# Kernel optimization log

Measured on AMD Instinct MI355X. Metric: run time of the kernel, lower is better.

Reference implementation:

```python
import jax, jax.numpy as jnp
import numpy as np
from math import sqrt

D = 512        # output_dim (layer_dims[-1])
H = 4          # num_heads
ATN = D // H   # atn_dim = 128
BERT_D = 768
B = 32         # number of graph pairs
NP = 4096
NH = 4096


def setup_inputs() -> dict:
    key = jax.random.key(0)
    ks = jax.random.split(key, 20)
    inp = {
        'ctx_p': jax.random.normal(ks[0], (NP, D), jnp.float32),
        'ctx_h': jax.random.normal(ks[1], (NH, D), jnp.float32),
        'lhs_p': jax.random.normal(ks[2], (NP, BERT_D), jnp.float32),
        'lhs_h': jax.random.normal(ks[3], (NH, BERT_D), jnp.float32),
        'batch_p': jnp.sort(jax.random.randint(ks[4], (NP,), 0, B)).astype(jnp.int64),
        'batch_h': jnp.sort(jax.random.randint(ks[5], (NH,), 0, B)).astype(jnp.int64),
        # learned parameters (stored [in, out])
        'Wq': jax.random.normal(ks[6], (D, D), jnp.float32) * 0.02,
        'bq': jnp.zeros((D,), jnp.float32),
        'Wk': jax.random.normal(ks[7], (D, D), jnp.float32) * 0.02,
        'bk': jnp.zeros((D,), jnp.float32),
        'Wv': jax.random.normal(ks[8], (BERT_D, BERT_D), jnp.float32) * 0.02,
        'bv': jnp.zeros((BERT_D,), jnp.float32),
        'W1': jax.random.normal(ks[9], (D + BERT_D, 256), jnp.float32) * 0.02,
        'b1': jnp.zeros((256,), jnp.float32),
        'W2': jax.random.normal(ks[10], (256, 128), jnp.float32) * 0.02,
        'ln_g': jnp.ones((128,), jnp.float32),
        'ln_b': jnp.zeros((128,), jnp.float32),
        'Wc': jax.random.normal(ks[11], (128, 3), jnp.float32) * 0.02,
        'bc': jnp.zeros((3,), jnp.float32),
    }
    return inp


def reference(ctx_p, ctx_h, lhs_p, lhs_h, batch_p, batch_h,
              Wq, bq, Wk, bk, Wv, bv, W1, b1, W2, ln_g, ln_b, Wc, bc):
    # q/k projections; torch code does .view(-1, atn_dim, num_heads) -> head is fastest axis
    qs = (ctx_h @ Wq + bq).reshape(-1, ATN, H)          # [nh, atn, H]
    ks = (ctx_p @ Wk + bk).reshape(-1, ATN, H)          # [np, atn, H]
    vs = (lhs_p @ Wv + bv).reshape(-1, H, BERT_D // H)  # [np, H, 768/H]

    atn = jnp.einsum('ndh,mdh->nmh', qs, ks) / sqrt(ATN)  # [nh, np, H]
    # faithful to original: positions where batch ids MATCH are set to -1e10
    mask_same = batch_h[:, None] == batch_p[None, :]       # [nh, np]
    atn = jnp.where(mask_same[:, :, None], jnp.float32(-1e10), atn)
    atn = jax.nn.softmax(atn, axis=1)                      # softmax over premise words m

    attended = jnp.einsum('nmh,mhd->nhd', atn, vs).reshape(-1, BERT_D)  # [nh, 768]

    feats = jnp.concatenate([ctx_h, lhs_h - attended], axis=1)  # [nh, D+768]
    h1 = jax.nn.gelu(feats @ W1 + b1, approximate=False)
    h2 = h1 @ W2                                                # Linear no bias
    mu = h2.mean(axis=-1, keepdims=True)
    var = ((h2 - mu) ** 2).mean(axis=-1, keepdims=True)
    h2 = (h2 - mu) * jax.lax.rsqrt(var + 1e-5) * ln_g + ln_b    # LayerNorm(128)

    # global_mean_pool over batch_h
    pooled = jax.ops.segment_sum(h2, batch_h, num_segments=B)
    counts = jax.ops.segment_sum(jnp.ones((h2.shape[0], 1), h2.dtype), batch_h, num_segments=B)
    pooled = pooled / jnp.maximum(counts, 1.0)

    return pooled @ Wc + bc  # [B, 3]
```

## Files before the change

kernel.cpp:

```cpp
#include <hip/hip_runtime.h>
#include <hip/hip_bf16.h>
#include <math.h>

#define NP_N 4096
#define NH_N 4096
#define D_N 512
#define BERT_N 768
#define H_N 4
#define B_N 32
#define SCL2 0.12754245006257576f

typedef __attribute__((ext_vector_type(8))) short short8;
typedef __attribute__((ext_vector_type(4))) float f32x4;
typedef __attribute__((ext_vector_type(4))) unsigned short ush4;
typedef __attribute__((ext_vector_type(4))) unsigned int uivec4;
typedef unsigned short ushort_t;

__device__ __forceinline__ void gl_lds16(const void* g, void* l) {
    __builtin_amdgcn_global_load_lds((const __attribute__((address_space(1))) void*)g,
                                     (__attribute__((address_space(3))) void*)l, 16, 0, 0);
}
__device__ __forceinline__ unsigned short f2bu(float f) {
    __hip_bfloat16 b = __float2bfloat16(f);
    return *reinterpret_cast<unsigned short*>(&b);
}
__device__ __forceinline__ float b2f(unsigned short u) {
    union { unsigned int i; float f; } x; x.i = ((unsigned int)u) << 16; return x.f;
}
__device__ __forceinline__ unsigned int pkbf(float a, float b) {
    union { __hip_bfloat162 h; unsigned int u; } x;
    x.h.x = __float2bfloat16(a);
    x.h.y = __float2bfloat16(b);
    return x.u;
}
__device__ __forceinline__ unsigned int sxor(unsigned int v, int m) {
    return (unsigned int)__shfl_xor((int)v, m);
}

__device__ __forceinline__ short8 mkfrag(uint2 u, uint2 v, bool hi, bool godd) {
    unsigned ux32 = sxor(u.x, 32), uy32 = sxor(u.y, 32);
    unsigned vx32 = sxor(v.x, 32), vy32 = sxor(v.y, 32);
    unsigned ax = hi ? vx32 : u.x, bx = hi ? v.x : ux32;
    unsigned ay = hi ? vy32 : u.y, by = hi ? v.y : uy32;
    unsigned sbx = sxor(bx, 16), sax = sxor(ax, 16);
    unsigned sby = sxor(by, 16), say = sxor(ay, 16);
    uivec4 w;
    w.x = godd ? sbx : ax;
    w.y = godd ? sby : ay;
    w.z = godd ? bx : sax;
    w.w = godd ? by : say;
    return __builtin_bit_cast(short8, w);
}

__global__ __launch_bounds__(256) void convert_all(
    const float* __restrict__ ctx_h, const float* __restrict__ ctx_p,
    const float* __restrict__ lhs_p,
    const float* __restrict__ Wq, const float* __restrict__ Wk,
    const float* __restrict__ Wv, const float* __restrict__ W1,
    const float* __restrict__ bq, const float* __restrict__ bk,
    ushort_t* __restrict__ ctxp_bf, ushort_t* __restrict__ lhsp_bf,
    ushort_t* __restrict__ feats,
    ushort_t* __restrict__ Wqt, ushort_t* __restrict__ Wkt,
    ushort_t* __restrict__ Wvt, ushort_t* __restrict__ W1t,
    float* __restrict__ bqp, float* __restrict__ bkp)
{
    const int bid = blockIdx.x, t = threadIdx.x;
    if (bid < 128) {
        for (long k = (long)bid * 256 + t; k < 524288; k += 128 * 256) {
            float4 v = ((const float4*)ctx_h)[k];
            ush4 o; o[0] = f2bu(v.x); o[1] = f2bu(v.y); o[2] = f2bu(v.z); o[3] = f2bu(v.w);
            long n = k >> 7, c4 = k & 127;
            ((ush4*)feats)[n * 320 + c4] = o;
        }
        if (bid == 0) {
            for (int n = t; n < 512; n += 256) {
                int np = (n & 3) * 128 + (n >> 2);
                bqp[np] = bq[n] * SCL2;
                bkp[np] = bk[n];
            }
        }
        return;
    }
    if (bid < 256) {
        for (long k = (long)(bid - 128) * 256 + t; k < 524288; k += 128 * 256) {
            float4 v = ((const float4*)ctx_p)[k];
            ush4 o; o[0] = f2bu(v.x); o[1] = f2bu(v.y); o[2] = f2bu(v.z); o[3] = f2bu(v.w);
            ((ush4*)ctxp_bf)[k] = o;
        }
        return;
    }
    if (bid < 448) {
        for (long k = (long)(bid - 256) * 256 + t; k < 786432; k += 192 * 256) {
            float4 v = ((const float4*)lhs_p)[k];
            ush4 o; o[0] = f2bu(v.x); o[1] = f2bu(v.y); o[2] = f2bu(v.z); o[3] = f2bu(v.w);
            ((ush4*)lhsp_bf)[k] = o;
        }
        return;
    }
    int tb = bid - 448;
    const float* src; ushort_t* dst; int K, N, tile, perm; float wscl;
    if (tb < 64)       { src = Wq; dst = Wqt; K = 512;  N = 512; tile = tb;       perm = 1; wscl = SCL2; }
    else if (tb < 128) { src = Wk; dst = Wkt; K = 512;  N = 512; tile = tb - 64;  perm = 1; wscl = 1.f; }
    else if (tb < 272) { src = Wv; dst = Wvt; K = 768;  N = 768; tile = tb - 128; perm = 0; wscl = 1.f; }
    else               { src = W1; dst = W1t; K = 1280; N = 256; tile = tb - 272; perm = 0; wscl = 1.f; }
    int ntn = N >> 6;
    int k0 = (tile / ntn) * 64, n0 = (tile % ntn) * 64;
    __shared__ float tl[64][65];
#pragma unroll
    for (int i = 0; i < 16; i++) {
        int idx = t + i * 256; int r = idx >> 6, c = idx & 63;
        tl[r][c] = src[(size_t)(k0 + r) * N + n0 + c];
    }
    __syncthreads();
#pragma unroll
    for (int i = 0; i < 16; i++) {
        int idx = t + i * 256; int r = idx >> 6, c = idx & 63;
        int n = n0 + r;
        int nr = perm ? ((n & 3) * 128 + (n >> 2)) : n;
        dst[(size_t)nr * K + k0 + c] = f2bu(tl[c][r] * wscl);
    }
}

__global__ __launch_bounds__(256, 2) void gemm_qkv(
    const ushort_t* __restrict__ feats, const ushort_t* __restrict__ ctxp,
    const ushort_t* __restrict__ Wqt, const ushort_t* __restrict__ Wkt,
    const ushort_t* __restrict__ Wvt, const ushort_t* __restrict__ lhsp,
    const float* __restrict__ bqp, const float* __restrict__ bkp,
    const float* __restrict__ bv,
    ushort_t* __restrict__ Qb, ushort_t* __restrict__ Kb,
    ushort_t* __restrict__ Vtb)
{
    int b = blockIdx.x;
    const ushort_t *A, *Bt; const float* bias; ushort_t* C;
    int lda, N, K, m0, n0, bias_row;
    if (b < 128) {
        A = feats; lda = 1280; Bt = Wqt; bias = bqp; C = Qb;
        N = 512; K = 512; bias_row = 0;
        n0 = (b & 3) * 128; m0 = (b >> 2) * 128;
    } else if (b < 256) {
        b -= 128;
        A = ctxp; lda = 512; Bt = Wkt; bias = bkp; C = Kb;
        N = 512; K = 512; bias_row = 0;
        n0 = (b & 3) * 128; m0 = (b >> 2) * 128;
    } else {
        b -= 256;
        A = Wvt; lda = 768; Bt = lhsp; bias = bv; C = Vtb;
        N = 4096; K = 768; bias_row = 1;
        n0 = (b & 31) * 128; m0 = (b >> 5) * 128;
    }
    const int nsteps = K >> 6;

    __shared__ ushort_t As[2][128 * 64];
    __shared__ ushort_t Bs[2][128 * 64];
    const int t = threadIdx.x, w = t >> 6, lane = t & 63;
    const int lq = lane & 15, g = lane >> 4;
    const int wm = w >> 1, wn = w & 1;

    f32x4 acc[4][4] = {};

    auto STAGE = [&](int buf, int k0) {
#pragma unroll
        for (int jj = 0; jj < 4; jj++) {
            int j = w * 4 + jj;
            int r = j * 8 + (lane >> 3);
            int c = ((lane & 7) * 16) ^ ((r & 7) << 4);
            gl_lds16((const char*)A + ((size_t)(m0 + r) * lda + k0) * 2 + c,
                     (void*)&As[buf][j * 512]);
            gl_lds16((const char*)Bt + ((size_t)(n0 + r) * K + k0) * 2 + c,
                     (void*)&Bs[buf][j * 512]);
        }
    };

    STAGE(0, 0);
    __syncthreads();
    int cur = 0;
    for (int s = 0; s < nsteps; s++) {
        if (s + 1 < nsteps) STAGE(cur ^ 1, (s + 1) * 64);
        const char* Ab = (const char*)&As[cur][0];
        const char* Bb = (const char*)&Bs[cur][0];
        const int swz = (lq & 7) << 4;
        short8 af[4][2], bfr[4][2];
#pragma unroll
        for (int mf = 0; mf < 4; mf++) {
            int r = wm * 64 + mf * 16 + lq;
#pragma unroll
            for (int ks = 0; ks < 2; ks++)
                af[mf][ks] = *(const short8*)(Ab + r * 128 + ((ks * 64 + g * 16) ^ swz));
        }
#pragma unroll
        for (int nf = 0; nf < 4; nf++) {
            int r = wn * 64 + nf * 16 + lq;
#pragma unroll
            for (int ks = 0; ks < 2; ks++)
                bfr[nf][ks] = *(const short8*)(Bb + r * 128 + ((ks * 64 + g * 16) ^ swz));
        }
        __builtin_amdgcn_s_setprio(1);
#pragma unroll
        for (int mf = 0; mf < 4; mf++)
#pragma unroll
            for (int nf = 0; nf < 4; nf++)
#pragma unroll
                for (int ks = 0; ks < 2; ks++)
                    acc[mf][nf] = __builtin_amdgcn_mfma_f32_16x16x32_bf16(
                        af[mf][ks], bfr[nf][ks], acc[mf][nf], 0, 0, 0);
        __builtin_amdgcn_s_setprio(0);
        __syncthreads();
        cur ^= 1;
    }

#pragma unroll
    for (int mf = 0; mf < 4; mf++) {
#pragma unroll
        for (int nf = 0; nf < 4; nf++) {
            int ncol = n0 + wn * 64 + nf * 16 + lq;
            float bcol = bias_row ? 0.f : bias[ncol];
#pragma unroll
            for (int j = 0; j < 4; j++) {
                int mrow = m0 + wm * 64 + mf * 16 + 4 * g + j;
                float v = acc[mf][nf][j] + (bias_row ? bias[mrow] : bcol);
                C[(size_t)mrow * N + ncol] = f2bu(v);
            }
        }
    }
}

__global__ __launch_bounds__(256) void gemm_mlp1(
    const ushort_t* __restrict__ A, int lda, const ushort_t* __restrict__ Bt,
    const float* __restrict__ bias, ushort_t* __restrict__ C,
    int M, int N, int K)
{
    __shared__ ushort_t As[2][64 * 64];
    __shared__ ushort_t Bs[2][64 * 64];
    const int t = threadIdx.x, w = t >> 6, lane = t & 63;
    const int lq = lane & 15, g = lane >> 4;
    const int wm = w >> 1, wn = w & 1;
    const int n0 = blockIdx.x * 64, m0 = blockIdx.y * 64;
    const int nsteps = K >> 6;

    f32x4 acc[2][2] = {};

    auto STAGE = [&](int buf, int k0) {
#pragma unroll
        for (int jj = 0; jj < 2; jj++) {
            int j = w * 2 + jj;
            int r = j * 8 + (lane >> 3);
            int c = ((lane & 7) * 16) ^ ((r & 7) << 4);
            gl_lds16((const char*)A + ((size_t)(m0 + r) * lda + k0) * 2 + c,
                     (void*)&As[buf][j * 512]);
            gl_lds16((const char*)Bt + ((size_t)(n0 + r) * K + k0) * 2 + c,
                     (void*)&Bs[buf][j * 512]);
        }
    };

    STAGE(0, 0);
    __syncthreads();
    int cur = 0;
    for (int s = 0; s < nsteps; s++) {
        if (s + 1 < nsteps) STAGE(cur ^ 1, (s + 1) * 64);
        const char* Ab = (const char*)&As[cur][0];
        const char* Bb = (const char*)&Bs[cur][0];
        const int swz = (lq & 7) << 4;
        short8 af[2][2], bfr[2][2];
#pragma unroll
        for (int mf = 0; mf < 2; mf++) {
            int r = wm * 32 + mf * 16 + lq;
#pragma unroll
            for (int ks = 0; ks < 2; ks++)
                af[mf][ks] = *(const short8*)(Ab + r * 128 + ((ks * 64 + g * 16) ^ swz));
        }
#pragma unroll
        for (int nf = 0; nf < 2; nf++) {
            int r = wn * 32 + nf * 16 + lq;
#pragma unroll
            for (int ks = 0; ks < 2; ks++)
                bfr[nf][ks] = *(const short8*)(Bb + r * 128 + ((ks * 64 + g * 16) ^ swz));
        }
#pragma unroll
        for (int mf = 0; mf < 2; mf++)
#pragma unroll
            for (int nf = 0; nf < 2; nf++)
#pragma unroll
                for (int ks = 0; ks < 2; ks++)
                    acc[mf][nf] = __builtin_amdgcn_mfma_f32_16x16x32_bf16(
                        af[mf][ks], bfr[nf][ks], acc[mf][nf], 0, 0, 0);
        __syncthreads();
        cur ^= 1;
    }

#pragma unroll
    for (int mf = 0; mf < 2; mf++) {
#pragma unroll
        for (int nf = 0; nf < 2; nf++) {
            int ncol = n0 + wn * 32 + nf * 16 + lq;
            float bcol = bias[ncol];
#pragma unroll
            for (int j = 0; j < 4; j++) {
                int mrow = m0 + wm * 32 + mf * 16 + 4 * g + j;
                float v = acc[mf][nf][j] + bcol;
                v = 0.5f * v * (1.f + erff(v * 0.70710678118654752f));
                C[(size_t)mrow * N + ncol] = f2bu(v);
            }
        }
    }
}

__global__ __launch_bounds__(256, 2) void attn_mfma(
    const ushort_t* __restrict__ Qb,
    const ushort_t* __restrict__ Kb,
    const ushort_t* __restrict__ Vtb,
    const int* __restrict__ batch_h, const int* __restrict__ batch_p,
    ushort_t* __restrict__ Opart,
    float* __restrict__ lsums)
{
    const int bid = blockIdx.x;
    const int h = (bid & 7) >> 1;
    const int outer = bid & 1;
    const int n0 = (bid >> 3) * 64;

    __shared__ __align__(16) char smem[81920];

    const int t = threadIdx.x;
    const int w = t >> 6;
    const int qc = w & 1;
    const int st = w >> 1;
    const int lane = t & 63, lq = lane & 15, g = lane >> 4;
    const int lqm = (lq & 7) << 4;
    const bool hi = lane >= 32;
    const bool godd = (lane & 16) != 0;

    char* base = smem + st * 40960;
    char* Kt0 = base;
    char* Kt1 = base + 8192;
    char* Vt0 = base + 16384;
    char* Vt1 = base + 28672;

    short8 qf[2][4];
    int bhq[2];
#pragma unroll
    for (int qg = 0; qg < 2; qg++) {
        const ushort_t* qrow = Qb + (size_t)(n0 + qc * 32 + qg * 16 + lq) * 512 + h * 128;
#pragma unroll
        for (int ks = 0; ks < 4; ks++)
            qf[qg][ks] = *(const short8*)(qrow + ks * 32 + g * 8);
        bhq[qg] = batch_h[n0 + qc * 32 + qg * 16 + lq];
    }

    f32x4 Ofr[2][12];
#pragma unroll
    for (int qg = 0; qg < 2; qg++)
#pragma unroll
        for (int nt = 0; nt < 12; nt++) Ofr[qg][nt] = (f32x4){0.f, 0.f, 0.f, 0.f};
    float l_run[2] = {0.f, 0.f};

    const char* Kg = (const char*)Kb;
    const char* Vg = (const char*)Vtb;
    const int kb = outer * 2048 + st * 1024;

    const int voff = ((lq >> 1) * 128) + ((((lq & 1) * 64) + g * 16) ^ (((lq >> 1) & 7) << 4));

    auto STAGE = [&](char* Kd, char* Vd, int m0k) {
#pragma unroll
        for (int jj = 0; jj < 4; jj++) {
            int j = qc * 4 + jj;
            int r = j * 4 + (lane >> 4);
            int c = ((lane & 15) * 16) ^ ((r & 7) << 4);
            gl_lds16(Kg + (size_t)(m0k + r) * 1024 + h * 256 + c, Kd + j * 1024);
        }
#pragma unroll
        for (int jj = 0; jj < 6; jj++) {
            int j = qc * 6 + jj;
            int rp = j * 8 + (lane >> 3);
            int inner = ((lane & 7) * 16) ^ ((rp & 7) << 4);
            int vd = rp * 2 + (inner >> 6);
            int kby = inner & 63;
            gl_lds16(Vg + ((size_t)(h * 192 + vd) * 4096 + m0k) * 2 + kby, Vd + j * 1024);
        }
    };

    STAGE(Kt0, Vt0, kb);
    asm volatile("s_waitcnt vmcnt(0)" ::: "memory");
    __builtin_amdgcn_s_barrier();
    int cur = 0;

    for (int tile = 0; tile < 32; tile++) {
        char* Kc = cur ? Kt1 : Kt0;
        char* Vc = cur ? Vt1 : Vt0;
        const int ktb = kb + tile * 32;

        int4 bp0 = *(const int4*)&batch_p[ktb + 4 * g];
        int4 bp1 = *(const int4*)&batch_p[ktb + 16 + 4 * g];

        if (tile + 1 < 32) STAGE(cur ? Kt0 : Kt1, cur ? Vt0 : Vt1, ktb + 32);

        f32x4 S[2][2];
#pragma unroll
        for (int qg = 0; qg < 2; qg++)
#pragma unroll
            for (int mt = 0; mt < 2; mt++) S[qg][mt] = (f32x4){0.f, 0.f, 0.f, 0.f};
        __builtin_amdgcn_s_setprio(1);
#pragma unroll
        for (int mt = 0; mt < 2; mt++) {
            const char* rbase = Kc + (mt * 16 + lq) * 256;
#pragma unroll
            for (int ks = 0; ks < 4; ks++) {
                short8 kf = *(const short8*)(rbase + ((ks * 64 + g * 16) ^ lqm));
                S[0][mt] = __builtin_amdgcn_mfma_f32_16x16x32_bf16(kf, qf[0][ks], S[0][mt], 0, 0, 0);
                S[1][mt] = __builtin_amdgcn_mfma_f32_16x16x32_bf16(kf, qf[1][ks], S[1][mt], 0, 0, 0);
            }
        }
        __builtin_amdgcn_s_setprio(0);

        uint2 P2[2][2];
#pragma unroll
        for (int qg = 0; qg < 2; qg++) {
            float e0 = (bp0.x == bhq[qg]) ? 0.f : exp2f(S[qg][0][0]);
            float e1 = (bp0.y == bhq[qg]) ? 0.f : exp2f(S[qg][0][1]);
            float e2 = (bp0.z == bhq[qg]) ? 0.f : exp2f(S[qg][0][2]);
            float e3 = (bp0.w == bhq[qg]) ? 0.f : exp2f(S[qg][0][3]);
            float f0 = (bp1.x == bhq[qg]) ? 0.f : exp2f(S[qg][1][0]);
            float f1 = (bp1.y == bhq[qg]) ? 0.f : exp2f(S[qg][1][1]);
            float f2 = (bp1.z == bhq[qg]) ? 0.f : exp2f(S[qg][1][2]);
            float f3 = (bp1.w == bhq[qg]) ? 0.f : exp2f(S[qg][1][3]);
            l_run[qg] += ((e0 + e1) + (e2 + e3)) + ((f0 + f1) + (f2 + f3));
            P2[qg][0].x = pkbf(e0, e1); P2[qg][0].y = pkbf(e2, e3);
            P2[qg][1].x = pkbf(f0, f1); P2[qg][1].y = pkbf(f2, f3);
        }

        short8 pf0 = mkfrag(P2[0][0], P2[0][1], hi, godd);
        short8 pf1 = mkfrag(P2[1][0], P2[1][1], hi, godd);
        __builtin_amdgcn_s_setprio(1);
#pragma unroll
        for (int nt = 0; nt < 12; nt++) {
            short8 vf = *(const short8*)(Vc + nt * 1024 + voff);
            Ofr[0][nt] = __builtin_amdgcn_mfma_f32_16x16x32_bf16(pf0, vf, Ofr[0][nt], 0, 0, 0);
            Ofr[1][nt] = __builtin_amdgcn_mfma_f32_16x16x32_bf16(pf1, vf, Ofr[1][nt], 0, 0, 0);
        }
        __builtin_amdgcn_s_setprio(0);

        asm volatile("s_waitcnt vmcnt(0)" ::: "memory");
        __builtin_amdgcn_s_barrier();
        cur ^= 1;
    }

    float lt[2];
#pragma unroll
    for (int qg = 0; qg < 2; qg++) {
        float l = l_run[qg];
        l += __shfl_xor(l, 16);
        l += __shfl_xor(l, 32);
        lt[qg] = l;
    }

    float* mO = (float*)smem;
    float* mls = (float*)(smem + 49152);
    if (st == 1) {
        float* dst = mO + ((size_t)qc * 64 + lane) * 96;
#pragma unroll
        for (int qg = 0; qg < 2; qg++) {
#pragma unroll
            for (int nt = 0; nt < 12; nt++)
                *(f32x4*)(dst + qg * 48 + nt * 4) = Ofr[qg][nt];
            if (g == 0) mls[(qc * 2 + qg) * 16 + lq] = lt[qg];
        }
    }
    __syncthreads();
    if (st == 0) {
        const float* srcO = mO + ((size_t)qc * 64 + lane) * 96;
        const size_t plane = (size_t)(outer * 4 + h) * 4096;
#pragma unroll
        for (int qg = 0; qg < 2; qg++) {
            int q0 = n0 + qc * 32 + qg * 16;
            if (g == 0)
                lsums[plane + q0 + lq] = lt[qg] + mls[(qc * 2 + qg) * 16 + lq];
#pragma unroll
            for (int nt = 0; nt < 12; nt++) {
                f32x4 o1 = *(const f32x4*)(srcO + qg * 48 + nt * 4);
#pragma unroll
                for (int j = 0; j < 4; j++)
                    Opart[(plane + q0 + 4 * g + j) * 192 + nt * 16 + lq] =
                        f2bu(Ofr[qg][nt][j] + o1[j]);
            }
        }
    }
}

__global__ __launch_bounds__(256) void combine_feats(
    const ushort_t* __restrict__ Opart, const float* __restrict__ lsums,
    const float* __restrict__ lhs_h, ushort_t* __restrict__ feats)
{
    const int t = threadIdx.x;
#pragma unroll
    for (int i = 0; i < 4; i++) {
        int q = blockIdx.x * 4 + i;
#pragma unroll
        for (int it = 0; it < 3; it++) {
            int c = t + it * 256;
            int h = c / 192, vd = c - h * 192;
            size_t i0 = (size_t)h * 4096 + q;
            size_t i1 = (size_t)(4 + h) * 4096 + q;
            float linv = 1.f / (lsums[i0] + lsums[i1]);
            float O = (b2f(Opart[i0 * 192 + vd]) + b2f(Opart[i1 * 192 + vd])) * linv;
            feats[(size_t)q * 1280 + 512 + c] = f2bu(lhs_h[(size_t)q * 768 + c] - O);
        }
    }
}

__global__ __launch_bounds__(256) void h2_ln(
    const ushort_t* __restrict__ h1, const float* __restrict__ W2,
    const float* __restrict__ ln_g, const float* __restrict__ ln_b,
    float* __restrict__ h2out)
{
    const int n0 = blockIdx.x * 8;
    const int t = threadIdx.x;
    __shared__ float h1s[8][256];
    __shared__ float h2s[8][128];

#pragma unroll
    for (int i = 0; i < 8; i++) {
        int idx = t + i * 256; int r = idx >> 8, c = idx & 255;
        h1s[r][c] = b2f(h1[(size_t)(n0 + r) * 256 + c]);
    }
    __syncthreads();

    {
        int o2 = t & 127, gq = t >> 7;
        float acc[4] = {};
        for (int k4 = 0; k4 < 64; k4++) {
            float w0 = W2[(size_t)(k4 * 4 + 0) * 128 + o2];
            float w1 = W2[(size_t)(k4 * 4 + 1) * 128 + o2];
            float w2 = W2[(size_t)(k4 * 4 + 2) * 128 + o2];
            float w3 = W2[(size_t)(k4 * 4 + 3) * 128 + o2];
#pragma unroll
            for (int q = 0; q < 4; q++) {
                float4 hh = *(const float4*)&h1s[gq * 4 + q][k4 * 4];
                acc[q] += hh.x * w0 + hh.y * w1 + hh.z * w2 + hh.w * w3;
            }
        }
#pragma unroll
        for (int q = 0; q < 4; q++) h2s[gq * 4 + q][o2] = acc[q];
    }
    __syncthreads();

    {
        int wv = t >> 6, lane = t & 63;
#pragma unroll
        for (int sx = 0; sx < 2; sx++) {
            int nd = wv * 2 + sx;
            float x0 = h2s[nd][lane], x1 = h2s[nd][lane + 64];
            float sum = x0 + x1;
#pragma unroll
            for (int off = 32; off; off >>= 1) sum += __shfl_xor(sum, off);
            float mu = sum * (1.f / 128.f);
            float d0 = x0 - mu, d1 = x1 - mu;
            float s2 = d0 * d0 + d1 * d1;
#pragma unroll
            for (int off = 32; off; off >>= 1) s2 += __shfl_xor(s2, off);
            float rstd = rsqrtf(s2 * (1.f / 128.f) + 1e-5f);
            size_t base = (size_t)(n0 + nd) * 128;
            h2out[base + lane]      = d0 * rstd * ln_g[lane] + ln_b[lane];
            h2out[base + lane + 64] = d1 * rstd * ln_g[lane + 64] + ln_b[lane + 64];
        }
    }
}

__global__ __launch_bounds__(128) void pool_cls(
    const float* __restrict__ h2, const int* __restrict__ batch_h,
    const float* __restrict__ Wc, const float* __restrict__ bc,
    float* __restrict__ out)
{
    int b = blockIdx.x, t = threadIdx.x;
    __shared__ int bounds[2];
    if (t < 2) {
        int target = b + t;
        int lo = 0, hi = NH_N;
        while (lo < hi) {
            int mid = (lo + hi) >> 1;
            if (batch_h[mid] < target) lo = mid + 1; else hi = mid;
        }
        bounds[t] = lo;
    }
    __syncthreads();
    int s = bounds[0], e = bounds[1];
    float acc = 0.f;
    for (int n = s; n < e; n++) acc += h2[(size_t)n * 128 + t];
    float pooled = acc / fmaxf((float)(e - s), 1.f);
    __shared__ float red[128];
    for (int c = 0; c < 3; c++) {
        red[t] = pooled * Wc[t * 3 + c];
        __syncthreads();
        for (int off = 64; off > 0; off >>= 1) {
            if (t < off) red[t] += red[t + off];
            __syncthreads();
        }
        if (t == 0) out[b * 3 + c] = red[0] + bc[c];
        __syncthreads();
    }
}

extern "C" void kernel_launch(void* const* d_in, const int* in_sizes, int n_in,
                              void* d_out, int out_size, void* d_ws, size_t ws_size,
                              hipStream_t stream)
{
    const float* ctx_p  = (const float*)d_in[0];
    const float* ctx_h  = (const float*)d_in[1];
    const float* lhs_p  = (const float*)d_in[2];
    const float* lhs_h  = (const float*)d_in[3];
    const int*   batch_p = (const int*)d_in[4];
    const int*   batch_h = (const int*)d_in[5];
    const float* Wq = (const float*)d_in[6];
    const float* bq = (const float*)d_in[7];
    const float* Wk = (const float*)d_in[8];
    const float* bk = (const float*)d_in[9];
    const float* Wv = (const float*)d_in[10];
    const float* bv = (const float*)d_in[11];
    const float* W1 = (const float*)d_in[12];
    const float* b1 = (const float*)d_in[13];
    const float* W2 = (const float*)d_in[14];
    const float* ln_g = (const float*)d_in[15];
    const float* ln_b = (const float*)d_in[16];
    const float* Wc = (const float*)d_in[17];
    const float* bc = (const float*)d_in[18];
    float* out = (float*)d_out;

    ushort_t* u = (ushort_t*)d_ws;
    ushort_t* ctxp_bf = u;
    ushort_t* lhsp_bf = ctxp_bf + 2097152;
    ushort_t* Wqt  = lhsp_bf + 3145728;
    ushort_t* Wkt  = Wqt + 262144;
    ushort_t* Wvt  = Wkt + 262144;
    ushort_t* Opart = u;
    ushort_t* W1t  = Wvt + 589824;
    ushort_t* Qb   = W1t + 327680;
    ushort_t* Kb   = Qb + 2097152;
    ushort_t* Vtb  = Kb + 2097152;
    ushort_t* feats = Vtb + 3145728;
    ushort_t* h1   = feats + 5242880;
    float* lsums = (float*)(h1 + 1048576);
    float* h2  = lsums + 65536;
    float* bqp = h2 + 524288;
    float* bkp = bqp + 512;

    convert_all<<<800, 256, 0, stream>>>(
        ctx_h, ctx_p, lhs_p, Wq, Wk, Wv, W1, bq, bk,
        ctxp_bf, lhsp_bf, feats, Wqt, Wkt, Wvt, W1t, bqp, bkp);

    gemm_qkv<<<448, 256, 0, stream>>>(
        feats, ctxp_bf, Wqt, Wkt, Wvt, lhsp_bf, bqp, bkp, bv, Qb, Kb, Vtb);

    attn_mfma<<<512, 256, 0, stream>>>(Qb, Kb, Vtb, batch_h, batch_p, Opart, lsums);

    combine_feats<<<1024, 256, 0, stream>>>(Opart, lsums, lhs_h, feats);

    gemm_mlp1<<<dim3(4, 64), 256, 0, stream>>>(feats, 1280, W1t, b1, h1, NH_N, 256, 1280);

    h2_ln<<<512, 256, 0, stream>>>(h1, W2, ln_g, ln_b, h2);
    pool_cls<<<B_N, 128, 0, stream>>>(h2, batch_h, Wc, bc, out);
}
```

Baseline: 194.0 us.

## Retile QKV GEMM to 64x64 and deepen attention K/V pipeline with larger blocks

The QKV projection GEMM moves from 128x128 to 64x64 tiles, launched as 1792 blocks instead of 448, which adds parallelism and lowers register and LDS pressure per block. The attention kernel now runs 512-thread blocks covering 128 queries. It keeps a triple-buffered K ring and a double-buffered V ring, issues the next tile's QK MFMA before the current softmax/PV step, and waits with a partial vmcnt so loads can overlap compute. The costs are more shared memory per block, more complex synchronisation with two barriers per tile, and more redundant operand loads in the smaller GEMM tiles.

```diff
diff --git a/kernel.cpp b/kernel.cpp
--- a/kernel.cpp
+++ b/kernel.cpp
@@ -121,7 +121,7 @@
     }
 }
 
-__global__ __launch_bounds__(256, 2) void gemm_qkv(
+__global__ __launch_bounds__(256) void gemm_qkv(
     const ushort_t* __restrict__ feats, const ushort_t* __restrict__ ctxp,
     const ushort_t* __restrict__ Wqt, const ushort_t* __restrict__ Wkt,
     const ushort_t* __restrict__ Wvt, const ushort_t* __restrict__ lhsp,
@@ -133,109 +133,28 @@
     int b = blockIdx.x;
     const ushort_t *A, *Bt; const float* bias; ushort_t* C;
     int lda, N, K, m0, n0, bias_row;
-    if (b < 128) {
+    if (b < 512) {
         A = feats; lda = 1280; Bt = Wqt; bias = bqp; C = Qb;
         N = 512; K = 512; bias_row = 0;
-        n0 = (b & 3) * 128; m0 = (b >> 2) * 128;
-    } else if (b < 256) {
-        b -= 128;
+        n0 = (b & 7) * 64; m0 = (b >> 3) * 64;
+    } else if (b < 1024) {
+        b -= 512;
         A = ctxp; lda = 512; Bt = Wkt; bias = bkp; C = Kb;
         N = 512; K = 512; bias_row = 0;
-        n0 = (b & 3) * 128; m0 = (b >> 2) * 128;
+        n0 = (b & 7) * 64; m0 = (b >> 3) * 64;
     } else {
-        b -= 256;
+        b -= 1024;
         A = Wvt; lda = 768; Bt = lhsp; bias = bv; C = Vtb;
         N = 4096; K = 768; bias_row = 1;
-        n0 = (b & 31) * 128; m0 = (b >> 5) * 128;
+        n0 = (b & 63) * 64; m0 = (b >> 6) * 64;
     }
     const int nsteps = K >> 6;
 
-    __shared__ ushort_t As[2][128 * 64];
-    __shared__ ushort_t Bs[2][128 * 64];
-    const int t = threadIdx.x, w = t >> 6, lane = t & 63;
-    const int lq = lane & 15, g = lane >> 4;
-    const int wm = w >> 1, wn = w & 1;
-
-    f32x4 acc[4][4] = {};
-
-    auto STAGE = [&](int buf, int k0) {
-#pragma unroll
-        for (int jj = 0; jj < 4; jj++) {
-            int j = w * 4 + jj;
-            int r = j * 8 + (lane >> 3);
-            int c = ((lane & 7) * 16) ^ ((r & 7) << 4);
-            gl_lds16((const char*)A + ((size_t)(m0 + r) * lda + k0) * 2 + c,
-                     (void*)&As[buf][j * 512]);
-            gl_lds16((const char*)Bt + ((size_t)(n0 + r) * K + k0) * 2 + c,
-                     (void*)&Bs[buf][j * 512]);
-        }
-    };
-
-    STAGE(0, 0);
-    __syncthreads();
-    int cur = 0;
-    for (int s = 0; s < nsteps; s++) {
-        if (s + 1 < nsteps) STAGE(cur ^ 1, (s + 1) * 64);
-        const char* Ab = (const char*)&As[cur][0];
-        const char* Bb = (const char*)&Bs[cur][0];
-        const int swz = (lq & 7) << 4;
-        short8 af[4][2], bfr[4][2];
-#pragma unroll
-        for (int mf = 0; mf < 4; mf++) {
-            int r = wm * 64 + mf * 16 + lq;
-#pragma unroll
-            for (int ks = 0; ks < 2; ks++)
-                af[mf][ks] = *(const short8*)(Ab + r * 128 + ((ks * 64 + g * 16) ^ swz));
-        }
-#pragma unroll
-        for (int nf = 0; nf < 4; nf++) {
-            int r = wn * 64 + nf * 16 + lq;
-#pragma unroll
-            for (int ks = 0; ks < 2; ks++)
-                bfr[nf][ks] = *(const short8*)(Bb + r * 128 + ((ks * 64 + g * 16) ^ swz));
-        }
-        __builtin_amdgcn_s_setprio(1);
-#pragma unroll
-        for (int mf = 0; mf < 4; mf++)
-#pragma unroll
-            for (int nf = 0; nf < 4; nf++)
-#pragma unroll
-                for (int ks = 0; ks < 2; ks++)
-                    acc[mf][nf] = __builtin_amdgcn_mfma_f32_16x16x32_bf16(
-                        af[mf][ks], bfr[nf][ks], acc[mf][nf], 0, 0, 0);
-        __builtin_amdgcn_s_setprio(0);
-        __syncthreads();
-        cur ^= 1;
-    }
-
-#pragma unroll
-    for (int mf = 0; mf < 4; mf++) {
-#pragma unroll
-        for (int nf = 0; nf < 4; nf++) {
-            int ncol = n0 + wn * 64 + nf * 16 + lq;
-            float bcol = bias_row ? 0.f : bias[ncol];
-#pragma unroll
-            for (int j = 0; j < 4; j++) {
-                int mrow = m0 + wm * 64 + mf * 16 + 4 * g + j;
-                float v = acc[mf][nf][j] + (bias_row ? bias[mrow] : bcol);
-                C[(size_t)mrow * N + ncol] = f2bu(v);
-            }
-        }
-    }
-}
-
-__global__ __launch_bounds__(256) void gemm_mlp1(
-    const ushort_t* __restrict__ A, int lda, const ushort_t* __restrict__ Bt,
-    const float* __restrict__ bias, ushort_t* __restrict__ C,
-    int M, int N, int K)
-{
     __shared__ ushort_t As[2][64 * 64];
     __shared__ ushort_t Bs[2][64 * 64];
     const int t = threadIdx.x, w = t >> 6, lane = t & 63;
     const int lq = lane & 15, g = lane >> 4;
     const int wm = w >> 1, wn = w & 1;
-    const int n0 = blockIdx.x * 64, m0 = blockIdx.y * 64;
-    const int nsteps = K >> 6;
 
     f32x4 acc[2][2] = {};
 
@@ -292,6 +211,85 @@
 #pragma unroll
         for (int nf = 0; nf < 2; nf++) {
             int ncol = n0 + wn * 32 + nf * 16 + lq;
+            float bcol = bias_row ? 0.f : bias[ncol];
+#pragma unroll
+            for (int j = 0; j < 4; j++) {
+                int mrow = m0 + wm * 32 + mf * 16 + 4 * g + j;
+                float v = acc[mf][nf][j] + (bias_row ? bias[mrow] : bcol);
+                C[(size_t)mrow * N + ncol] = f2bu(v);
+            }
+        }
+    }
+}
+
+__global__ __launch_bounds__(256) void gemm_mlp1(
+    const ushort_t* __restrict__ A, int lda, const ushort_t* __restrict__ Bt,
+    const float* __restrict__ bias, ushort_t* __restrict__ C,
+    int M, int N, int K)
+{
+    __shared__ ushort_t As[2][64 * 64];
+    __shared__ ushort_t Bs[2][64 * 64];
+    const int t = threadIdx.x, w = t >> 6, lane = t & 63;
+    const int lq = lane & 15, g = lane >> 4;
+    const int wm = w >> 1, wn = w & 1;
+    const int n0 = blockIdx.x * 64, m0 = blockIdx.y * 64;
+    const int nsteps = K >> 6;
+
+    f32x4 acc[2][2] = {};
+
+    auto STAGE = [&](int buf, int k0) {
+#pragma unroll
+        for (int jj = 0; jj < 2; jj++) {
+            int j = w * 2 + jj;
+            int r = j * 8 + (lane >> 3);
+            int c = ((lane & 7) * 16) ^ ((r & 7) << 4);
+            gl_lds16((const char*)A + ((size_t)(m0 + r) * lda + k0) * 2 + c,
+                     (void*)&As[buf][j * 512]);
+            gl_lds16((const char*)Bt + ((size_t)(n0 + r) * K + k0) * 2 + c,
+                     (void*)&Bs[buf][j * 512]);
+        }
+    };
+
+    STAGE(0, 0);
+    __syncthreads();
+    int cur = 0;
+    for (int s = 0; s < nsteps; s++) {
+        if (s + 1 < nsteps) STAGE(cur ^ 1, (s + 1) * 64);
+        const char* Ab = (const char*)&As[cur][0];
+        const char* Bb = (const char*)&Bs[cur][0];
+        const int swz = (lq & 7) << 4;
+        short8 af[2][2], bfr[2][2];
+#pragma unroll
+        for (int mf = 0; mf < 2; mf++) {
+            int r = wm * 32 + mf * 16 + lq;
+#pragma unroll
+            for (int ks = 0; ks < 2; ks++)
+                af[mf][ks] = *(const short8*)(Ab + r * 128 + ((ks * 64 + g * 16) ^ swz));
+        }
+#pragma unroll
+        for (int nf = 0; nf < 2; nf++) {
+            int r = wn * 32 + nf * 16 + lq;
+#pragma unroll
+            for (int ks = 0; ks < 2; ks++)
+                bfr[nf][ks] = *(const short8*)(Bb + r * 128 + ((ks * 64 + g * 16) ^ swz));
+        }
+#pragma unroll
+        for (int mf = 0; mf < 2; mf++)
+#pragma unroll
+            for (int nf = 0; nf < 2; nf++)
+#pragma unroll
+                for (int ks = 0; ks < 2; ks++)
+                    acc[mf][nf] = __builtin_amdgcn_mfma_f32_16x16x32_bf16(
+                        af[mf][ks], bfr[nf][ks], acc[mf][nf], 0, 0, 0);
+        __syncthreads();
+        cur ^= 1;
+    }
+
+#pragma unroll
+    for (int mf = 0; mf < 2; mf++) {
+#pragma unroll
+        for (int nf = 0; nf < 2; nf++) {
+            int ncol = n0 + wn * 32 + nf * 16 + lq;
             float bcol = bias[ncol];
 #pragma unroll
             for (int j = 0; j < 4; j++) {
@@ -304,7 +302,7 @@
     }
 }
 
-__global__ __launch_bounds__(256, 2) void attn_mfma(
+__global__ __launch_bounds__(512, 2) void attn_mfma(
     const ushort_t* __restrict__ Qb,
     const ushort_t* __restrict__ Kb,
     const ushort_t* __restrict__ Vtb,
@@ -315,24 +313,22 @@
     const int bid = blockIdx.x;
     const int h = (bid & 7) >> 1;
     const int outer = bid & 1;
-    const int n0 = (bid >> 3) * 64;
-
-    __shared__ __align__(16) char smem[81920];
+    const int n0 = (bid >> 3) * 128;
+
+    __shared__ __align__(16) char smem[99328];
 
     const int t = threadIdx.x;
     const int w = t >> 6;
-    const int qc = w & 1;
-    const int st = w >> 1;
+    const int st = w & 1;
+    const int qc = w >> 1;
     const int lane = t & 63, lq = lane & 15, g = lane >> 4;
     const int lqm = (lq & 7) << 4;
     const bool hi = lane >= 32;
     const bool godd = (lane & 16) != 0;
 
-    char* base = smem + st * 40960;
-    char* Kt0 = base;
-    char* Kt1 = base + 8192;
-    char* Vt0 = base + 16384;
-    char* Vt1 = base + 28672;
+    char* base = smem + st * 49152;
+    char* ksl[3] = { base, base + 8192, base + 16384 };
+    char* vsl[2] = { base + 24576, base + 36864 };
 
     short8 qf[2][4];
     int bhq[2];
@@ -358,46 +354,31 @@
 
     const int voff = ((lq >> 1) * 128) + ((((lq & 1) * 64) + g * 16) ^ (((lq >> 1) & 7) << 4));
 
-    auto STAGE = [&](char* Kd, char* Vd, int m0k) {
-#pragma unroll
-        for (int jj = 0; jj < 4; jj++) {
-            int j = qc * 4 + jj;
+    auto STAGE_K = [&](char* Kd, int key0) {
+#pragma unroll
+        for (int jj = 0; jj < 2; jj++) {
+            int j = qc * 2 + jj;
             int r = j * 4 + (lane >> 4);
             int c = ((lane & 15) * 16) ^ ((r & 7) << 4);
-            gl_lds16(Kg + (size_t)(m0k + r) * 1024 + h * 256 + c, Kd + j * 1024);
-        }
-#pragma unroll
-        for (int jj = 0; jj < 6; jj++) {
-            int j = qc * 6 + jj;
+            gl_lds16(Kg + (size_t)(key0 + r) * 1024 + h * 256 + c, Kd + j * 1024);
+        }
+    };
+    auto STAGE_V = [&](char* Vd, int key0) {
+#pragma unroll
+        for (int jj = 0; jj < 3; jj++) {
+            int j = qc * 3 + jj;
             int rp = j * 8 + (lane >> 3);
             int inner = ((lane & 7) * 16) ^ ((rp & 7) << 4);
             int vd = rp * 2 + (inner >> 6);
             int kby = inner & 63;
-            gl_lds16(Vg + ((size_t)(h * 192 + vd) * 4096 + m0k) * 2 + kby, Vd + j * 1024);
+            gl_lds16(Vg + ((size_t)(h * 192 + vd) * 4096 + key0) * 2 + kby, Vd + j * 1024);
         }
     };
-
-    STAGE(Kt0, Vt0, kb);
-    asm volatile("s_waitcnt vmcnt(0)" ::: "memory");
-    __builtin_amdgcn_s_barrier();
-    int cur = 0;
-
-    for (int tile = 0; tile < 32; tile++) {
-        char* Kc = cur ? Kt1 : Kt0;
-        char* Vc = cur ? Vt1 : Vt0;
-        const int ktb = kb + tile * 32;
-
-        int4 bp0 = *(const int4*)&batch_p[ktb + 4 * g];
-        int4 bp1 = *(const int4*)&batch_p[ktb + 16 + 4 * g];
-
-        if (tile + 1 < 32) STAGE(cur ? Kt0 : Kt1, cur ? Vt0 : Vt1, ktb + 32);
-
-        f32x4 S[2][2];
+    auto QK = [&](const char* Kc, f32x4 (&S)[2][2]) {
 #pragma unroll
         for (int qg = 0; qg < 2; qg++)
 #pragma unroll
             for (int mt = 0; mt < 2; mt++) S[qg][mt] = (f32x4){0.f, 0.f, 0.f, 0.f};
-        __builtin_amdgcn_s_setprio(1);
 #pragma unroll
         for (int mt = 0; mt < 2; mt++) {
             const char* rbase = Kc + (mt * 16 + lq) * 256;
@@ -408,19 +389,35 @@
                 S[1][mt] = __builtin_amdgcn_mfma_f32_16x16x32_bf16(kf, qf[1][ks], S[1][mt], 0, 0, 0);
             }
         }
-        __builtin_amdgcn_s_setprio(0);
+    };
+
+    STAGE_K(ksl[0], kb);      STAGE_V(vsl[0], kb);
+    STAGE_K(ksl[1], kb + 32); STAGE_V(vsl[1], kb + 32);
+    STAGE_K(ksl[2], kb + 64);
+    asm volatile("s_waitcnt vmcnt(0)" ::: "memory");
+    __builtin_amdgcn_s_barrier();
+
+    int4 bp0 = *(const int4*)&batch_p[kb + 4 * g];
+    int4 bp1 = *(const int4*)&batch_p[kb + 16 + 4 * g];
+
+    f32x4 SA[2][2], SB[2][2];
+    QK(ksl[0], SA);
+
+    auto BODY = [&](int tt, f32x4 (&SC)[2][2], f32x4 (&SN)[2][2]) {
+        const int tp1 = tt + 1;
+        if (tp1 < 32) QK(ksl[tp1 % 3], SN);
 
         uint2 P2[2][2];
 #pragma unroll
         for (int qg = 0; qg < 2; qg++) {
-            float e0 = (bp0.x == bhq[qg]) ? 0.f : exp2f(S[qg][0][0]);
-            float e1 = (bp0.y == bhq[qg]) ? 0.f : exp2f(S[qg][0][1]);
-            float e2 = (bp0.z == bhq[qg]) ? 0.f : exp2f(S[qg][0][2]);
-            float e3 = (bp0.w == bhq[qg]) ? 0.f : exp2f(S[qg][0][3]);
-            float f0 = (bp1.x == bhq[qg]) ? 0.f : exp2f(S[qg][1][0]);
-            float f1 = (bp1.y == bhq[qg]) ? 0.f : exp2f(S[qg][1][1]);
-            float f2 = (bp1.z == bhq[qg]) ? 0.f : exp2f(S[qg][1][2]);
-            float f3 = (bp1.w == bhq[qg]) ? 0.f : exp2f(S[qg][1][3]);
+            float e0 = (bp0.x == bhq[qg]) ? 0.f : exp2f(SC[qg][0][0]);
+            float e1 = (bp0.y == bhq[qg]) ? 0.f : exp2f(SC[qg][0][1]);
+            float e2 = (bp0.z == bhq[qg]) ? 0.f : exp2f(SC[qg][0][2]);
+            float e3 = (bp0.w == bhq[qg]) ? 0.f : exp2f(SC[qg][0][3]);
+            float f0 = (bp1.x == bhq[qg]) ? 0.f : exp2f(SC[qg][1][0]);
+            float f1 = (bp1.y == bhq[qg]) ? 0.f : exp2f(SC[qg][1][1]);
+            float f2 = (bp1.z == bhq[qg]) ? 0.f : exp2f(SC[qg][1][2]);
+            float f3 = (bp1.w == bhq[qg]) ? 0.f : exp2f(SC[qg][1][3]);
             l_run[qg] += ((e0 + e1) + (e2 + e3)) + ((f0 + f1) + (f2 + f3));
             P2[qg][0].x = pkbf(e0, e1); P2[qg][0].y = pkbf(e2, e3);
             P2[qg][1].x = pkbf(f0, f1); P2[qg][1].y = pkbf(f2, f3);
@@ -428,6 +425,7 @@
 
         short8 pf0 = mkfrag(P2[0][0], P2[0][1], hi, godd);
         short8 pf1 = mkfrag(P2[1][0], P2[1][1], hi, godd);
+        const char* Vc = vsl[tt & 1];
         __builtin_amdgcn_s_setprio(1);
 #pragma unroll
         for (int nt = 0; nt < 12; nt++) {
@@ -437,9 +435,21 @@
         }
         __builtin_amdgcn_s_setprio(0);
 
-        asm volatile("s_waitcnt vmcnt(0)" ::: "memory");
         __builtin_amdgcn_s_barrier();
-        cur ^= 1;
+        if (tt + 3 < 32) STAGE_K(ksl[tt % 3], kb + (tt + 3) * 32);
+        if (tt + 2 < 32) STAGE_V(vsl[tt & 1], kb + (tt + 2) * 32);
+        if (tt < 29) { asm volatile("s_waitcnt vmcnt(5)" ::: "memory"); }
+        else         { asm volatile("s_waitcnt vmcnt(0)" ::: "memory"); }
+        __builtin_amdgcn_s_barrier();
+        if (tp1 < 32) {
+            bp0 = *(const int4*)&batch_p[kb + tp1 * 32 + 4 * g];
+            bp1 = *(const int4*)&batch_p[kb + tp1 * 32 + 16 + 4 * g];
+        }
+    };
+
+    for (int tt = 0; tt < 32; tt += 2) {
+        BODY(tt, SA, SB);
+        BODY(tt + 1, SB, SA);
     }
 
     float lt[2];
@@ -452,7 +462,7 @@
     }
 
     float* mO = (float*)smem;
-    float* mls = (float*)(smem + 49152);
+    float* mls = (float*)(smem + 98304);
     if (st == 1) {
         float* dst = mO + ((size_t)qc * 64 + lane) * 96;
 #pragma unroll
@@ -644,10 +654,10 @@
         ctx_h, ctx_p, lhs_p, Wq, Wk, Wv, W1, bq, bk,
         ctxp_bf, lhsp_bf, feats, Wqt, Wkt, Wvt, W1t, bqp, bkp);
 
-    gemm_qkv<<<448, 256, 0, stream>>>(
+    gemm_qkv<<<1792, 256, 0, stream>>>(
         feats, ctxp_bf, Wqt, Wkt, Wvt, lhsp_bf, bqp, bkp, bv, Qb, Kb, Vtb);
 
-    attn_mfma<<<512, 256, 0, stream>>>(Qb, Kb, Vtb, batch_h, batch_p, Opart, lsums);
+    attn_mfma<<<256, 512, 0, stream>>>(Qb, Kb, Vtb, batch_h, batch_p, Opart, lsums);
 
     combine_feats<<<1024, 256, 0, stream>>>(Opart, lsums, lhs_h, feats);
 
```

New measurement: 215.3 us. 1.11x slower.
